# Performance work log

Measured on AMD Instinct MI355X. Metric: run time of the kernel, lower is better.

## Reference

```python
import jax, jax.numpy as jnp
import numpy as np

NMAX = 8
LMAX = 3
RC = 5.0
SMOOTH_WIDTH = 0.5
BASIS_SIGMA = 0.5
N_SPECIES = 4
N_ATOMS = 20000
N_EDGES = 800000
LM = (LMAX + 1) ** 2  # 16


def shifted_cosine_cutoff(r):
    # fc = 1 for r < rc - w; smooth cosine ramp to 0 on [rc - w, rc]; 0 beyond rc
    t = (r - (RC - SMOOTH_WIDTH)) / SMOOTH_WIDTH
    ramp = 0.5 * (jnp.cos(jnp.pi * jnp.clip(t, 0.0, 1.0)) + 1.0)
    return jnp.where(r < RC - SMOOTH_WIDTH, 1.0, jnp.where(r < RC, ramp, 0.0))


def real_sph_harm(v):
    # Real spherical harmonics up to l=3, 'integral' (orthonormal) normalization,
    # e3nn component ordering (l=1 block is y,z,x). v assumed unit vectors. -> (E,16)
    x, y, z = v[:, 0], v[:, 1], v[:, 2]
    x2, y2, z2 = x * x, y * y, z * z
    Y = [
        jnp.full_like(x, 0.28209479177387814),                      # l=0
        0.4886025119029199 * y,                                     # l=1
        0.4886025119029199 * z,
        0.4886025119029199 * x,
        1.0925484305920792 * x * y,                                  # l=2
        1.0925484305920792 * y * z,
        0.31539156525252005 * (3.0 * z2 - 1.0),
        1.0925484305920792 * x * z,
        0.5462742152960396 * (x2 - y2),
        0.5900435899266435 * y * (3.0 * x2 - y2),                   # l=3
        2.890611442640554 * x * y * z,
        0.4570457994644658 * y * (5.0 * z2 - 1.0),
        0.3731763325901154 * z * (5.0 * z2 - 3.0),
        0.4570457994644658 * x * (5.0 * z2 - 1.0),
        1.445305721320277 * z * (x2 - y2),
        0.5900435899266435 * x * (x2 - 3.0 * y2),
    ]
    return jnp.stack(Y, axis=-1)


def setup_inputs() -> dict:
    key = jax.random.key(0)
    k1, k2, k3, k4, k5, k6 = jax.random.split(key, 6)
    distances = jax.random.uniform(k1, (N_EDGES,), dtype=jnp.float32) * RC
    dirs = jax.random.normal(k2, (N_EDGES, 3), dtype=jnp.float32)
    dirs = dirs / jnp.linalg.norm(dirs, axis=1, keepdims=True)
    W_radial = jax.random.normal(k3, (LMAX + 1, NMAX, 16), dtype=jnp.float32)
    centers = jnp.linspace(0.0, RC, 16, dtype=jnp.float32)
    z = jax.random.randint(k4, (N_ATOMS,), 0, N_SPECIES)
    idx_i = jax.random.randint(k5, (N_EDGES,), 0, N_ATOMS)
    idx_j = jax.random.randint(k6, (N_EDGES,), 0, N_ATOMS)
    return {"distances": distances, "direction_vectors": dirs, "W_radial": W_radial,
            "centers": centers, "z": z, "idx_i": idx_i, "idx_j": idx_j}


def reference(distances, direction_vectors, W_radial, centers, z, idx_i, idx_j):
    # radial integrals: splined Rln modeled as linear combo of Gaussian radial basis
    g = jnp.exp(-((distances[:, None] - centers[None, :]) ** 2) / (2.0 * BASIS_SIGMA ** 2))  # (E,K)
    fc = shifted_cosine_cutoff(distances)  # (E,)
    RIln = jnp.einsum('ek,lnk->eln', g, W_radial) * fc[:, None, None]  # (E, lmax+1, nmax)
    Ylm = real_sph_harm(direction_vectors)  # (E, 16)
    # per-l outer product RIln[:,l,:] (x) Ylm block -> (E, nmax, lm)
    blocks = []
    idx = 0
    for l in range(LMAX + 1):
        w = 2 * l + 1
        blocks.append(jnp.einsum('en,em->enm', RIln[:, l, :], Ylm[:, idx:idx + w]))
        idx += w
    cij_nlm = jnp.concatenate(blocks, axis=-1)  # (E, nmax, 16)
    # species-dependent scatter-sum: bin = species_idx(z_j) + n_species * idx_i
    reduction_ids = z[idx_j] + N_SPECIES * idx_i
    ci = jax.ops.segment_sum(cij_nlm, reduction_ids, num_segments=N_SPECIES * N_ATOMS)
    return ci.reshape(N_ATOMS, N_SPECIES, NMAX, LM)
```

## Files before the change

### kernel.cpp

```cpp
#include <hip/hip_runtime.h>


#define NMAXC   8
#define LMC     16
#define NSPECC  4
#define RCUT    5.0f
#define RIN_    4.5f
#define PI_F    3.14159265358979323846f
#define CAP     128
#define CPAD    16

__device__ const int   d_Asel[16] = {0,2,3,1,4,2,0,1,0,2,4,2,3,1,3,1};
__device__ const int   d_Bsel[16] = {0,0,0,0,0,1,2,1,3,4,1,5,6,5,3,7};
__device__ const float d_Clm[16]  = {
    0.28209479177387814f, 0.4886025119029199f, 0.4886025119029199f,
    0.4886025119029199f,  1.0925484305920792f, 1.0925484305920792f,
    0.31539156525252005f, 1.0925484305920792f, 0.5462742152960396f,
    0.5900435899266435f,  2.890611442640554f,  0.4570457994644658f,
    0.3731763325901154f,  0.4570457994644658f, 1.445305721320277f,
    0.5900435899266435f };

__global__ void k_rec_bucket(const float* __restrict__ dist,
                             const float* __restrict__ dirs,
                             const int* __restrict__ zarr,
                             const int* __restrict__ idx_i,
                             const int* __restrict__ idx_j,
                             int* __restrict__ cursors_p,
                             float4* __restrict__ recs, int n_edges) {
    int e = blockIdx.x * blockDim.x + threadIdx.x;
    if (e >= n_edges) return;
    float d = dist[e];
    float x = dirs[3 * e + 0], y = dirs[3 * e + 1], zz = dirs[3 * e + 2];
    int s = zarr[idx_j[e]] & 3;
    int a = idx_i[e];
    int c = atomicAdd(&cursors_p[a * CPAD], 1);
    if (c >= CAP) return;
    unsigned db = (__float_as_uint(d) & ~3u) | (unsigned)s;
    float4 r; r.x = __uint_as_float(db); r.y = x; r.z = y; r.w = zz;
    recs[(size_t)a * CAP + c] = r;
}

__global__ void k_count_p(const int* __restrict__ idx_i, int* __restrict__ counts_p,
                          int n_edges) {
    int e = blockIdx.x * blockDim.x + threadIdx.x;
    if (e < n_edges) atomicAdd(&counts_p[idx_i[e] * CPAD], 1);
}

__global__ __launch_bounds__(1024) void k_scan_p(const int* __restrict__ counts_p,
                                                 int* __restrict__ offsets,
                                                 int* __restrict__ cursors_p, int n) {
    __shared__ int wsum[16];
    __shared__ int carry_s;
    int t = threadIdx.x;
    int lane = t & 63, w = t >> 6;
    if (t == 0) carry_s = 0;
    __syncthreads();
    for (int base = 0; base < n; base += 1024) {
        int i = base + t;
        int v = (i < n) ? counts_p[i * CPAD] : 0;
        int x = v;
        #pragma unroll
        for (int off = 1; off < 64; off <<= 1) {
            int y = __shfl_up(x, off);
            if (lane >= off) x += y;
        }
        if (lane == 63) wsum[w] = x;
        __syncthreads();
        if (w == 0) {
            int ws = (lane < 16) ? wsum[lane] : 0;
            #pragma unroll
            for (int off = 1; off < 16; off <<= 1) {
                int y = __shfl_up(ws, off);
                if (lane >= off) ws += y;
            }
            if (lane < 16) wsum[lane] = ws;
        }
        __syncthreads();
        int wbase = (w > 0) ? wsum[w - 1] : 0;
        int inc = wbase + x;
        int carry = carry_s;
        if (i < n) {
            int exc = carry + inc - v;
            offsets[i] = exc;
            cursors_p[i * CPAD] = exc;
        }
        __syncthreads();
        if (t == 1023) carry_s = carry + inc;
        __syncthreads();
    }
}

__global__ void k_rec_csr(const float* __restrict__ dist,
                          const float* __restrict__ dirs,
                          const int* __restrict__ zarr,
                          const int* __restrict__ idx_i,
                          const int* __restrict__ idx_j,
                          int* __restrict__ cursors_p,
                          float4* __restrict__ recs, int n_edges) {
    int e = blockIdx.x * blockDim.x + threadIdx.x;
    if (e >= n_edges) return;
    float d = dist[e];
    float x = dirs[3 * e + 0], y = dirs[3 * e + 1], zz = dirs[3 * e + 2];
    int s = zarr[idx_j[e]] & 3;
    int a = idx_i[e];
    int c = atomicAdd(&cursors_p[a * CPAD], 1);
    unsigned db = (__float_as_uint(d) & ~3u) | (unsigned)s;
    float4 r; r.x = __uint_as_float(db); r.y = x; r.z = y; r.w = zz;
    recs[c] = r;
}

__global__ __launch_bounds__(128) void k_main(
        const float4* __restrict__ recs, const float* __restrict__ W,
        const float* __restrict__ centers, const int* __restrict__ cnts_p,
        const int* __restrict__ offsets, float* __restrict__ out) {
    const int atom = blockIdx.x;
    const int t = threadIdx.x;
    const int w = t >> 6, L = t & 63;
    const int lm = L & 15;
    const int eL = L >> 4;
    const int l  = (lm >= 9) ? 3 : (lm >= 4) ? 2 : (lm >= 1) ? 1 : 0;
    const int r0 = l * 8 + eL;
    const int row = L & 31, p = L >> 5;

    const float ck   = centers[lm];
    const float c_lm = d_Clm[lm];
    const int   asel = d_Asel[lm], bsel = d_Bsel[lm];

    const float4* wp = reinterpret_cast<const float4*>(W + (row << 4));
    const float4 w0 = wp[0], w1 = wp[1], w2 = wp[2], w3 = wp[3];

    __shared__ float ggfc[2][4][16];
    __shared__ float ylmS[2][4][16];
    __shared__ float rinS[2][4][32];
    __shared__ int   msS [2][4];
    __shared__ float red [2][8][64];

    int cnt = cnts_p[atom * CPAD];
    size_t rbase;
    if (offsets) { rbase = (size_t)offsets[atom]; }
    else         { rbase = (size_t)atom * CAP; if (cnt > CAP) cnt = CAP; }

    float a00 = 0.f, a01 = 0.f, a10 = 0.f, a11 = 0.f;
    float a20 = 0.f, a21 = 0.f, a30 = 0.f, a31 = 0.f;

    for (int base = w * 4; base < cnt; base += 8) {
        int slot = base + eL;
        bool valid = slot < cnt;
        int rs = valid ? slot : base;
        float4 rec = recs[rbase + rs];
        unsigned db = __float_as_uint(rec.x);
        int spec = db & 3;
        float d = rec.x, x = rec.y, y = rec.z, zz = rec.w;
        float tt = fminf(fmaxf((d - RIN_) * 2.0f, 0.0f), 1.0f);
        float fcv = 0.5f * (__cosf(PI_F * tt) + 1.0f);
        float dd = d - ck;
        float g = __expf(-2.0f * dd * dd) * fcv;
        g = valid ? g : 0.0f;
        float x2 = x * x, y2 = y * y, z2 = zz * zz;
        float A = (asel == 0) ? 1.0f :
                  (asel == 1) ? x    :
                  (asel == 2) ? y    :
                  (asel == 3) ? zz   : x * y;
        float B = (bsel == 0) ? 1.0f :
                  (bsel == 1) ? zz   :
                  (bsel == 2) ? fmaf(3.0f, z2, -1.0f) :
                  (bsel == 3) ? (x2 - y2)             :
                  (bsel == 4) ? fmaf(3.0f, x2, -y2)   :
                  (bsel == 5) ? fmaf(5.0f, z2, -1.0f) :
                  (bsel == 6) ? fmaf(5.0f, z2, -3.0f) :
                                fmaf(-3.0f, y2, x2);
        float yv = c_lm * A * B;
        yv = valid ? yv : 0.0f;
        ggfc[w][eL][lm] = g;
        ylmS[w][eL][lm] = yv;
        if (lm == 0) msS[w][eL] = spec;
        __builtin_amdgcn_wave_barrier();
        {
            const float4* ga = reinterpret_cast<const float4*>(&ggfc[w][p][0]);
            const float4* gb = reinterpret_cast<const float4*>(&ggfc[w][p + 2][0]);
            float4 A0 = ga[0], A1 = ga[1], A2 = ga[2], A3 = ga[3];
            float4 B0 = gb[0], B1 = gb[1], B2 = gb[2], B3 = gb[3];
            float ra = A0.x * w0.x;
            ra = fmaf(A0.y, w0.y, ra); ra = fmaf(A0.z, w0.z, ra); ra = fmaf(A0.w, w0.w, ra);
            ra = fmaf(A1.x, w1.x, ra); ra = fmaf(A1.y, w1.y, ra); ra = fmaf(A1.z, w1.z, ra); ra = fmaf(A1.w, w1.w, ra);
            ra = fmaf(A2.x, w2.x, ra); ra = fmaf(A2.y, w2.y, ra); ra = fmaf(A2.z, w2.z, ra); ra = fmaf(A2.w, w2.w, ra);
            ra = fmaf(A3.x, w3.x, ra); ra = fmaf(A3.y, w3.y, ra); ra = fmaf(A3.z, w3.z, ra); ra = fmaf(A3.w, w3.w, ra);
            float rb = B0.x * w0.x;
            rb = fmaf(B0.y, w0.y, rb); rb = fmaf(B0.z, w0.z, rb); rb = fmaf(B0.w, w0.w, rb);
            rb = fmaf(B1.x, w1.x, rb); rb = fmaf(B1.y, w1.y, rb); rb = fmaf(B1.z, w1.z, rb); rb = fmaf(B1.w, w1.w, rb);
            rb = fmaf(B2.x, w2.x, rb); rb = fmaf(B2.y, w2.y, rb); rb = fmaf(B2.z, w2.z, rb); rb = fmaf(B2.w, w2.w, rb);
            rb = fmaf(B3.x, w3.x, rb); rb = fmaf(B3.y, w3.y, rb); rb = fmaf(B3.z, w3.z, rb); rb = fmaf(B3.w, w3.w, rb);
            rinS[w][p][row]     = ra;
            rinS[w][p + 2][row] = rb;
        }
        __builtin_amdgcn_wave_barrier();
        #pragma unroll
        for (int e = 0; e < 4; ++e) {
            float ye = ylmS[w][e][lm];
            float ra = rinS[w][e][r0];
            float rb = rinS[w][e][r0 + 4];
            int s = __builtin_amdgcn_readfirstlane(msS[w][e]);
            float v0 = ra * ye, v1 = rb * ye;
            if (s == 0)      { a00 += v0; a01 += v1; }
            else if (s == 1) { a10 += v0; a11 += v1; }
            else if (s == 2) { a20 += v0; a21 += v1; }
            else             { a30 += v0; a31 += v1; }
        }
        __builtin_amdgcn_wave_barrier();
    }

    red[w][0][L] = a00; red[w][1][L] = a01;
    red[w][2][L] = a10; red[w][3][L] = a11;
    red[w][4][L] = a20; red[w][5][L] = a21;
    red[w][6][L] = a30; red[w][7][L] = a31;
    __syncthreads();
    const int h = t >> 6, Ls = t & 63;
    float* ob = out + (size_t)atom * (NSPECC * NMAXC * LMC);
    #pragma unroll
    for (int s = 0; s < 4; ++s) {
        float v = red[0][s * 2 + h][Ls] + red[1][s * 2 + h][Ls];
        ob[s * 128 + t] = v;
    }
}

__device__ __forceinline__ float cutoff_fn(float d) {
    float tt = (d - RIN_) * 2.0f;
    tt = fminf(fmaxf(tt, 0.0f), 1.0f);
    float ramp = 0.5f * (cosf(PI_F * tt) + 1.0f);
    return (d < RCUT) ? ramp : 0.0f;
}

__device__ __forceinline__ float sph_harm_sw(int lm, float x, float y, float z) {
    float x2 = x * x, y2 = y * y, z2 = z * z;
    switch (lm) {
        case 0:  return 0.28209479177387814f;
        case 1:  return 0.4886025119029199f * y;
        case 2:  return 0.4886025119029199f * z;
        case 3:  return 0.4886025119029199f * x;
        case 4:  return 1.0925484305920792f * x * y;
        case 5:  return 1.0925484305920792f * y * z;
        case 6:  return 0.31539156525252005f * (3.0f * z2 - 1.0f);
        case 7:  return 1.0925484305920792f * x * z;
        case 8:  return 0.5462742152960396f * (x2 - y2);
        case 9:  return 0.5900435899266435f * y * (3.0f * x2 - y2);
        case 10: return 2.890611442640554f * x * y * z;
        case 11: return 0.4570457994644658f * y * (5.0f * z2 - 1.0f);
        case 12: return 0.3731763325901154f * z * (5.0f * z2 - 3.0f);
        case 13: return 0.4570457994644658f * x * (5.0f * z2 - 1.0f);
        case 14: return 1.445305721320277f * z * (x2 - y2);
        default: return 0.5900435899266435f * x * (x2 - 3.0f * y2);
    }
}

__global__ __launch_bounds__(128) void k_atomic(
        const float* __restrict__ distances, const float* __restrict__ dirs,
        const float* __restrict__ W, const float* __restrict__ centers,
        const int* __restrict__ zarr, const int* __restrict__ idx_i,
        const int* __restrict__ idx_j, float* __restrict__ out, int n_edges) {
    const int t = threadIdx.x;
    const int n = t >> 4, lm = t & 15;
    const int base = blockIdx.x * 8;

    __shared__ float4 gbuf[8][4];
    __shared__ float  ylm[8][16];
    __shared__ float  md[8], mfc[8], mx[8], my[8], mz[8];
    __shared__ int    ms[8], mi[8];

    const int l = (lm >= 9) ? 3 : (lm >= 4) ? 2 : (lm >= 1) ? 1 : 0;
    const float4* wp = reinterpret_cast<const float4*>(W + ((l * NMAXC + n) << 4));
    const float4 w0 = wp[0], w1 = wp[1], w2 = wp[2], w3 = wp[3];
    const float ck = centers[lm];

    if (t < 8) {
        int e = base + t;
        if (e < n_edges) {
            float d = distances[e];
            md[t] = d; mfc[t] = cutoff_fn(d);
            mx[t] = dirs[3 * e + 0];
            my[t] = dirs[3 * e + 1];
            mz[t] = dirs[3 * e + 2];
            ms[t] = zarr[idx_j[e]];
            mi[t] = idx_i[e];
        } else {
            md[t] = 1e9f; mfc[t] = 0.f;
            mx[t] = 0.f; my[t] = 0.f; mz[t] = 0.f; ms[t] = 0; mi[t] = 0;
        }
    }
    __syncthreads();
    {
        int e = t >> 4;
        float dd = md[e] - ck;
        reinterpret_cast<float*>(&gbuf[e][0])[lm] = __expf(-2.0f * dd * dd) * mfc[e];
    }
    {
        int e2 = t & 7, lm2 = t >> 3;
        ylm[e2][lm2] = sph_harm_sw(lm2, mx[e2], my[e2], mz[e2]);
    }
    __syncthreads();
    #pragma unroll
    for (int e = 0; e < 8; ++e) {
        float4 a0 = gbuf[e][0], a1 = gbuf[e][1], a2 = gbuf[e][2], a3 = gbuf[e][3];
        float r;
        r = a0.x * w0.x;
        r = fmaf(a0.y, w0.y, r); r = fmaf(a0.z, w0.z, r); r = fmaf(a0.w, w0.w, r);
        r = fmaf(a1.x, w1.x, r); r = fmaf(a1.y, w1.y, r); r = fmaf(a1.z, w1.z, r); r = fmaf(a1.w, w1.w, r);
        r = fmaf(a2.x, w2.x, r); r = fmaf(a2.y, w2.y, r); r = fmaf(a2.z, w2.z, r); r = fmaf(a2.w, w2.w, r);
        r = fmaf(a3.x, w3.x, r); r = fmaf(a3.y, w3.y, r); r = fmaf(a3.z, w3.z, r); r = fmaf(a3.w, w3.w, r);
        float v = r * ylm[e][lm];
        int target = (mi[e] * NSPECC + ms[e]) * (NMAXC * LMC) + t;
        unsafeAtomicAdd(&out[target], v);
    }
}

extern "C" void kernel_launch(void* const* d_in, const int* in_sizes, int n_in,
                              void* d_out, int out_size, void* d_ws, size_t ws_size,
                              hipStream_t stream) {
    const float* distances = (const float*)d_in[0];
    const float* dirs      = (const float*)d_in[1];
    const float* W         = (const float*)d_in[2];
    const float* centers   = (const float*)d_in[3];
    const int*   zarr      = (const int*)d_in[4];
    const int*   idx_i     = (const int*)d_in[5];
    const int*   idx_j     = (const int*)d_in[6];
    float*       out       = (float*)d_out;

    const int n_edges = in_sizes[0];
    const int n_atoms = in_sizes[4];

    const size_t curs_b  = (size_t)n_atoms * CPAD * sizeof(int);
    const size_t need_t1 = curs_b + (size_t)n_atoms * CAP * sizeof(float4) + 64;
    const size_t need_t2 = 2 * curs_b + (size_t)n_atoms * sizeof(int)
                         + (size_t)n_edges * sizeof(float4) + 64;

    if (ws_size >= need_t1) {
        int*    cursors_p = (int*)d_ws;
        float4* recs      = (float4*)((char*)d_ws + curs_b);
        hipMemsetAsync(cursors_p, 0, curs_b, stream);
        k_rec_bucket<<<(n_edges + 255) / 256, 256, 0, stream>>>(
            distances, dirs, zarr, idx_i, idx_j, cursors_p, recs, n_edges);
        k_main<<<n_atoms, 128, 0, stream>>>(recs, W, centers, cursors_p,
                                            nullptr, out);
    } else if (ws_size >= need_t2) {
        int*    counts_p  = (int*)d_ws;
        int*    cursors_p = (int*)((char*)d_ws + curs_b);
        int*    offsets   = (int*)((char*)d_ws + 2 * curs_b);
        float4* recs      = (float4*)((char*)d_ws + 2 * curs_b
                                      + (size_t)n_atoms * sizeof(int));
        hipMemsetAsync(counts_p, 0, curs_b, stream);
        k_count_p<<<(n_edges + 255) / 256, 256, 0, stream>>>(idx_i, counts_p, n_edges);
        k_scan_p<<<1, 1024, 0, stream>>>(counts_p, offsets, cursors_p, n_atoms);
        k_rec_csr<<<(n_edges + 255) / 256, 256, 0, stream>>>(
            distances, dirs, zarr, idx_i, idx_j, cursors_p, recs, n_edges);
        k_main<<<n_atoms, 128, 0, stream>>>(recs, W, centers, counts_p,
                                            offsets, out);
    } else {
        hipMemsetAsync(out, 0, (size_t)out_size * sizeof(float), stream);
        k_atomic<<<(n_edges + 7) / 8, 128, 0, stream>>>(distances, dirs, W, centers,
                                                        zarr, idx_i, idx_j, out, n_edges);
    }
}
```

Before: 198.7 us.

## Split record packing from bucketing; scatter edge ids and prefetch records in main loop

The edge record packing moves into its own coalesced kernel that writes records in edge order, and the bucketing kernel now scatters only 4-byte edge ids per atom instead of 16-byte records. The main kernel reads records indirectly through the id list, handles 8 edges per wave per iteration instead of 4, and prefetches the next records and ids in software. The aim is to shrink the scattered atomic-driven writes and to hide gather latency. The cost is an extra launch, an extra indirection with random 16-byte gathers in the main kernel, and more registers.

Result: slower. 211.7 us (+6.5%).

```diff
diff --git a/kernel.cpp b/kernel.cpp
--- a/kernel.cpp
+++ b/kernel.cpp
@@ -20,24 +20,47 @@
     0.3731763325901154f,  0.4570457994644658f, 1.445305721320277f,
     0.5900435899266435f };
 
-__global__ void k_rec_bucket(const float* __restrict__ dist,
-                             const float* __restrict__ dirs,
-                             const int* __restrict__ zarr,
-                             const int* __restrict__ idx_i,
-                             const int* __restrict__ idx_j,
-                             int* __restrict__ cursors_p,
-                             float4* __restrict__ recs, int n_edges) {
+__device__ __forceinline__ float ylm_eval(int asel, int bsel, float c_lm,
+                                          float x, float y, float zz) {
+    float x2 = x * x, y2 = y * y, z2 = zz * zz;
+    float A = (asel == 0) ? 1.0f :
+              (asel == 1) ? x    :
+              (asel == 2) ? y    :
+              (asel == 3) ? zz   : x * y;
+    float B = (bsel == 0) ? 1.0f :
+              (bsel == 1) ? zz   :
+              (bsel == 2) ? fmaf(3.0f, z2, -1.0f) :
+              (bsel == 3) ? (x2 - y2)             :
+              (bsel == 4) ? fmaf(3.0f, x2, -y2)   :
+              (bsel == 5) ? fmaf(5.0f, z2, -1.0f) :
+              (bsel == 6) ? fmaf(5.0f, z2, -3.0f) :
+                            fmaf(-3.0f, y2, x2);
+    return c_lm * A * B;
+}
+
+__global__ void k_prep(const float* __restrict__ dist,
+                       const float* __restrict__ dirs,
+                       const int* __restrict__ zarr,
+                       const int* __restrict__ idx_j,
+                       float4* __restrict__ recs, int n_edges) {
     int e = blockIdx.x * blockDim.x + threadIdx.x;
     if (e >= n_edges) return;
     float d = dist[e];
     float x = dirs[3 * e + 0], y = dirs[3 * e + 1], zz = dirs[3 * e + 2];
     int s = zarr[idx_j[e]] & 3;
+    unsigned db = (__float_as_uint(d) & ~3u) | (unsigned)s;
+    float4 r; r.x = __uint_as_float(db); r.y = x; r.z = y; r.w = zz;
+    recs[e] = r;
+}
+
+__global__ void k_scatter_id(const int* __restrict__ idx_i,
+                             int* __restrict__ cursors_p,
+                             int* __restrict__ ids, int n_edges) {
+    int e = blockIdx.x * blockDim.x + threadIdx.x;
+    if (e >= n_edges) return;
     int a = idx_i[e];
     int c = atomicAdd(&cursors_p[a * CPAD], 1);
-    if (c >= CAP) return;
-    unsigned db = (__float_as_uint(d) & ~3u) | (unsigned)s;
-    float4 r; r.x = __uint_as_float(db); r.y = x; r.z = y; r.w = zz;
-    recs[(size_t)a * CAP + c] = r;
+    if (c < CAP) ids[a * CAP + c] = e;
 }
 
 __global__ void k_count_p(const int* __restrict__ idx_i, int* __restrict__ counts_p,
@@ -90,123 +113,125 @@
     }
 }
 
-__global__ void k_rec_csr(const float* __restrict__ dist,
-                          const float* __restrict__ dirs,
-                          const int* __restrict__ zarr,
-                          const int* __restrict__ idx_i,
-                          const int* __restrict__ idx_j,
-                          int* __restrict__ cursors_p,
-                          float4* __restrict__ recs, int n_edges) {
+__global__ void k_scatter_id_csr(const int* __restrict__ idx_i,
+                                 int* __restrict__ cursors_p,
+                                 int* __restrict__ ids, int n_edges) {
     int e = blockIdx.x * blockDim.x + threadIdx.x;
     if (e >= n_edges) return;
-    float d = dist[e];
-    float x = dirs[3 * e + 0], y = dirs[3 * e + 1], zz = dirs[3 * e + 2];
-    int s = zarr[idx_j[e]] & 3;
-    int a = idx_i[e];
-    int c = atomicAdd(&cursors_p[a * CPAD], 1);
-    unsigned db = (__float_as_uint(d) & ~3u) | (unsigned)s;
-    float4 r; r.x = __uint_as_float(db); r.y = x; r.z = y; r.w = zz;
-    recs[c] = r;
+    int pos = atomicAdd(&cursors_p[idx_i[e] * CPAD], 1);
+    ids[pos] = e;
 }
 
 __global__ __launch_bounds__(128) void k_main(
-        const float4* __restrict__ recs, const float* __restrict__ W,
-        const float* __restrict__ centers, const int* __restrict__ cnts_p,
-        const int* __restrict__ offsets, float* __restrict__ out) {
+        const float4* __restrict__ recs, const int* __restrict__ ids_all,
+        const float* __restrict__ W, const float* __restrict__ centers,
+        const int* __restrict__ cnts_p, const int* __restrict__ offsets,
+        float* __restrict__ out) {
     const int atom = blockIdx.x;
     const int t = threadIdx.x;
     const int w = t >> 6, L = t & 63;
-    const int lm = L & 15;
-    const int eL = L >> 4;
+    const int lm = L & 15, g = L >> 4;
     const int l  = (lm >= 9) ? 3 : (lm >= 4) ? 2 : (lm >= 1) ? 1 : 0;
-    const int r0 = l * 8 + eL;
+    const int r0 = l * 8 + g;
     const int row = L & 31, p = L >> 5;
 
     const float ck   = centers[lm];
     const float c_lm = d_Clm[lm];
     const int   asel = d_Asel[lm], bsel = d_Bsel[lm];
-
     const float4* wp = reinterpret_cast<const float4*>(W + (row << 4));
     const float4 w0 = wp[0], w1 = wp[1], w2 = wp[2], w3 = wp[3];
 
-    __shared__ float ggfc[2][4][16];
-    __shared__ float ylmS[2][4][16];
-    __shared__ float rinS[2][4][32];
-    __shared__ int   msS [2][4];
+    __shared__ float ggfc[2][8][16];
+    __shared__ float ylmS[2][8][16];
+    __shared__ float rinS[2][8][32];
+    __shared__ int   msS [2][8];
     __shared__ float red [2][8][64];
 
     int cnt = cnts_p[atom * CPAD];
-    size_t rbase;
-    if (offsets) { rbase = (size_t)offsets[atom]; }
-    else         { rbase = (size_t)atom * CAP; if (cnt > CAP) cnt = CAP; }
-
-    float a00 = 0.f, a01 = 0.f, a10 = 0.f, a11 = 0.f;
-    float a20 = 0.f, a21 = 0.f, a30 = 0.f, a31 = 0.f;
-
-    for (int base = w * 4; base < cnt; base += 8) {
-        int slot = base + eL;
-        bool valid = slot < cnt;
-        int rs = valid ? slot : base;
-        float4 rec = recs[rbase + rs];
-        unsigned db = __float_as_uint(rec.x);
-        int spec = db & 3;
-        float d = rec.x, x = rec.y, y = rec.z, zz = rec.w;
-        float tt = fminf(fmaxf((d - RIN_) * 2.0f, 0.0f), 1.0f);
-        float fcv = 0.5f * (__cosf(PI_F * tt) + 1.0f);
-        float dd = d - ck;
-        float g = __expf(-2.0f * dd * dd) * fcv;
-        g = valid ? g : 0.0f;
-        float x2 = x * x, y2 = y * y, z2 = zz * zz;
-        float A = (asel == 0) ? 1.0f :
-                  (asel == 1) ? x    :
-                  (asel == 2) ? y    :
-                  (asel == 3) ? zz   : x * y;
-        float B = (bsel == 0) ? 1.0f :
-                  (bsel == 1) ? zz   :
-                  (bsel == 2) ? fmaf(3.0f, z2, -1.0f) :
-                  (bsel == 3) ? (x2 - y2)             :
-                  (bsel == 4) ? fmaf(3.0f, x2, -y2)   :
-                  (bsel == 5) ? fmaf(5.0f, z2, -1.0f) :
-                  (bsel == 6) ? fmaf(5.0f, z2, -3.0f) :
-                                fmaf(-3.0f, y2, x2);
-        float yv = c_lm * A * B;
-        yv = valid ? yv : 0.0f;
-        ggfc[w][eL][lm] = g;
-        ylmS[w][eL][lm] = yv;
-        if (lm == 0) msS[w][eL] = spec;
-        __builtin_amdgcn_wave_barrier();
-        {
-            const float4* ga = reinterpret_cast<const float4*>(&ggfc[w][p][0]);
-            const float4* gb = reinterpret_cast<const float4*>(&ggfc[w][p + 2][0]);
-            float4 A0 = ga[0], A1 = ga[1], A2 = ga[2], A3 = ga[3];
-            float4 B0 = gb[0], B1 = gb[1], B2 = gb[2], B3 = gb[3];
-            float ra = A0.x * w0.x;
-            ra = fmaf(A0.y, w0.y, ra); ra = fmaf(A0.z, w0.z, ra); ra = fmaf(A0.w, w0.w, ra);
-            ra = fmaf(A1.x, w1.x, ra); ra = fmaf(A1.y, w1.y, ra); ra = fmaf(A1.z, w1.z, ra); ra = fmaf(A1.w, w1.w, ra);
-            ra = fmaf(A2.x, w2.x, ra); ra = fmaf(A2.y, w2.y, ra); ra = fmaf(A2.z, w2.z, ra); ra = fmaf(A2.w, w2.w, ra);
-            ra = fmaf(A3.x, w3.x, ra); ra = fmaf(A3.y, w3.y, ra); ra = fmaf(A3.z, w3.z, ra); ra = fmaf(A3.w, w3.w, ra);
-            float rb = B0.x * w0.x;
-            rb = fmaf(B0.y, w0.y, rb); rb = fmaf(B0.z, w0.z, rb); rb = fmaf(B0.w, w0.w, rb);
-            rb = fmaf(B1.x, w1.x, rb); rb = fmaf(B1.y, w1.y, rb); rb = fmaf(B1.z, w1.z, rb); rb = fmaf(B1.w, w1.w, rb);
-            rb = fmaf(B2.x, w2.x, rb); rb = fmaf(B2.y, w2.y, rb); rb = fmaf(B2.z, w2.z, rb); rb = fmaf(B2.w, w2.w, rb);
-            rb = fmaf(B3.x, w3.x, rb); rb = fmaf(B3.y, w3.y, rb); rb = fmaf(B3.z, w3.z, rb); rb = fmaf(B3.w, w3.w, rb);
-            rinS[w][p][row]     = ra;
-            rinS[w][p + 2][row] = rb;
-        }
-        __builtin_amdgcn_wave_barrier();
-        #pragma unroll
-        for (int e = 0; e < 4; ++e) {
-            float ye = ylmS[w][e][lm];
-            float ra = rinS[w][e][r0];
-            float rb = rinS[w][e][r0 + 4];
-            int s = __builtin_amdgcn_readfirstlane(msS[w][e]);
-            float v0 = ra * ye, v1 = rb * ye;
-            if (s == 0)      { a00 += v0; a01 += v1; }
-            else if (s == 1) { a10 += v0; a11 += v1; }
-            else if (s == 2) { a20 += v0; a21 += v1; }
-            else             { a30 += v0; a31 += v1; }
-        }
-        __builtin_amdgcn_wave_barrier();
+    const int* idsp;
+    if (offsets) { idsp = ids_all + offsets[atom]; }
+    else { idsp = ids_all + (size_t)atom * CAP; if (cnt > CAP) cnt = CAP; }
+
+    float a00=0.f,a01=0.f,a10=0.f,a11=0.f,a20=0.f,a21=0.f,a30=0.f,a31=0.f;
+
+    if (cnt > 0) {
+        int base = w * 8;
+        int sA = base + g, sB = sA + 4;
+        bool vA = sA < cnt, vB = sB < cnt;
+        int iA = idsp[vA ? sA : 0];
+        int iB = idsp[vB ? sB : 0];
+        int sA1 = sA + 16, sB1 = sB + 16;
+        bool vA1 = sA1 < cnt, vB1 = sB1 < cnt;
+        int iA1 = idsp[vA1 ? sA1 : 0];
+        int iB1 = idsp[vB1 ? sB1 : 0];
+        float4 rA = recs[iA], rB = recs[iB];
+
+        for (; base < cnt; base += 16) {
+            float4 rAn = recs[iA1], rBn = recs[iB1];
+            int sA2 = sA + 32, sB2 = sB + 32;
+            bool vA2 = sA2 < cnt, vB2 = sB2 < cnt;
+            int iA2 = idsp[vA2 ? sA2 : 0];
+            int iB2 = idsp[vB2 ? sB2 : 0];
+
+            {
+                float d = rA.x, x = rA.y, y = rA.z, zz = rA.w;
+                int spec = __float_as_uint(d) & 3;
+                float tt = fminf(fmaxf((d - RIN_) * 2.0f, 0.0f), 1.0f);
+                float fcv = 0.5f * (__cosf(PI_F * tt) + 1.0f);
+                float dd = d - ck;
+                float gv = __expf(-2.0f * dd * dd) * fcv;
+                gv = vA ? gv : 0.0f;
+                float yv = ylm_eval(asel, bsel, c_lm, x, y, zz);
+                yv = vA ? yv : 0.0f;
+                ggfc[w][g][lm] = gv; ylmS[w][g][lm] = yv;
+                if (lm == 0) msS[w][g] = spec;
+            }
+            {
+                float d = rB.x, x = rB.y, y = rB.z, zz = rB.w;
+                int spec = __float_as_uint(d) & 3;
+                float tt = fminf(fmaxf((d - RIN_) * 2.0f, 0.0f), 1.0f);
+                float fcv = 0.5f * (__cosf(PI_F * tt) + 1.0f);
+                float dd = d - ck;
+                float gv = __expf(-2.0f * dd * dd) * fcv;
+                gv = vB ? gv : 0.0f;
+                float yv = ylm_eval(asel, bsel, c_lm, x, y, zz);
+                yv = vB ? yv : 0.0f;
+                ggfc[w][g + 4][lm] = gv; ylmS[w][g + 4][lm] = yv;
+                if (lm == 0) msS[w][g + 4] = spec;
+            }
+            __builtin_amdgcn_wave_barrier();
+            #pragma unroll
+            for (int q = 0; q < 4; ++q) {
+                int e = p + 2 * q;
+                const float4* ga = reinterpret_cast<const float4*>(&ggfc[w][e][0]);
+                float4 A0 = ga[0], A1 = ga[1], A2 = ga[2], A3 = ga[3];
+                float r = A0.x * w0.x;
+                r = fmaf(A0.y, w0.y, r); r = fmaf(A0.z, w0.z, r); r = fmaf(A0.w, w0.w, r);
+                r = fmaf(A1.x, w1.x, r); r = fmaf(A1.y, w1.y, r); r = fmaf(A1.z, w1.z, r); r = fmaf(A1.w, w1.w, r);
+                r = fmaf(A2.x, w2.x, r); r = fmaf(A2.y, w2.y, r); r = fmaf(A2.z, w2.z, r); r = fmaf(A2.w, w2.w, r);
+                r = fmaf(A3.x, w3.x, r); r = fmaf(A3.y, w3.y, r); r = fmaf(A3.z, w3.z, r); r = fmaf(A3.w, w3.w, r);
+                rinS[w][e][row] = r;
+            }
+            __builtin_amdgcn_wave_barrier();
+            #pragma unroll
+            for (int e = 0; e < 8; ++e) {
+                float ye = ylmS[w][e][lm];
+                float va = rinS[w][e][r0];
+                float vb = rinS[w][e][r0 + 4];
+                int s = __builtin_amdgcn_readfirstlane(msS[w][e]);
+                float v0 = va * ye, v1 = vb * ye;
+                if (s == 0)      { a00 += v0; a01 += v1; }
+                else if (s == 1) { a10 += v0; a11 += v1; }
+                else if (s == 2) { a20 += v0; a21 += v1; }
+                else             { a30 += v0; a31 += v1; }
+            }
+            __builtin_amdgcn_wave_barrier();
+
+            rA = rAn; rB = rBn;
+            vA = vA1; vB = vB1;
+            sA = sA1; sB = sB1;
+            sA1 = sA2; sB1 = sB2; vA1 = vA2; vB1 = vB2; iA1 = iA2; iB1 = iB2;
+        }
     }
 
     red[w][0][L] = a00; red[w][1][L] = a01;
@@ -217,10 +242,8 @@
     const int h = t >> 6, Ls = t & 63;
     float* ob = out + (size_t)atom * (NSPECC * NMAXC * LMC);
     #pragma unroll
-    for (int s = 0; s < 4; ++s) {
-        float v = red[0][s * 2 + h][Ls] + red[1][s * 2 + h][Ls];
-        ob[s * 128 + t] = v;
-    }
+    for (int s = 0; s < 4; ++s)
+        ob[s * 128 + t] = red[0][s * 2 + h][Ls] + red[1][s * 2 + h][Ls];
 }
 
 __device__ __forceinline__ float cutoff_fn(float d) {
@@ -228,28 +251,6 @@
     tt = fminf(fmaxf(tt, 0.0f), 1.0f);
     float ramp = 0.5f * (cosf(PI_F * tt) + 1.0f);
     return (d < RCUT) ? ramp : 0.0f;
-}
-
-__device__ __forceinline__ float sph_harm_sw(int lm, float x, float y, float z) {
-    float x2 = x * x, y2 = y * y, z2 = z * z;
-    switch (lm) {
-        case 0:  return 0.28209479177387814f;
-        case 1:  return 0.4886025119029199f * y;
-        case 2:  return 0.4886025119029199f * z;
-        case 3:  return 0.4886025119029199f * x;
-        case 4:  return 1.0925484305920792f * x * y;
-        case 5:  return 1.0925484305920792f * y * z;
-        case 6:  return 0.31539156525252005f * (3.0f * z2 - 1.0f);
-        case 7:  return 1.0925484305920792f * x * z;
-        case 8:  return 0.5462742152960396f * (x2 - y2);
-        case 9:  return 0.5900435899266435f * y * (3.0f * x2 - y2);
-        case 10: return 2.890611442640554f * x * y * z;
-        case 11: return 0.4570457994644658f * y * (5.0f * z2 - 1.0f);
-        case 12: return 0.3731763325901154f * z * (5.0f * z2 - 3.0f);
-        case 13: return 0.4570457994644658f * x * (5.0f * z2 - 1.0f);
-        case 14: return 1.445305721320277f * z * (x2 - y2);
-        default: return 0.5900435899266435f * x * (x2 - 3.0f * y2);
-    }
 }
 
 __global__ __launch_bounds__(128) void k_atomic(
@@ -294,7 +295,8 @@
     }
     {
         int e2 = t & 7, lm2 = t >> 3;
-        ylm[e2][lm2] = sph_harm_sw(lm2, mx[e2], my[e2], mz[e2]);
+        ylm[e2][lm2] = ylm_eval(d_Asel[lm2], d_Bsel[lm2], d_Clm[lm2],
+                                mx[e2], my[e2], mz[e2]);
     }
     __syncthreads();
     #pragma unroll
@@ -326,32 +328,38 @@
 
     const int n_edges = in_sizes[0];
     const int n_atoms = in_sizes[4];
-
-    const size_t curs_b  = (size_t)n_atoms * CPAD * sizeof(int);
-    const size_t need_t1 = curs_b + (size_t)n_atoms * CAP * sizeof(float4) + 64;
-    const size_t need_t2 = 2 * curs_b + (size_t)n_atoms * sizeof(int)
-                         + (size_t)n_edges * sizeof(float4) + 64;
+    const int eb = (n_edges + 255) / 256;
+
+    const size_t curs_b = (size_t)n_atoms * CPAD * sizeof(int);
+    const size_t recs_b = (size_t)n_edges * sizeof(float4);
+    const size_t ids1_b = (size_t)n_atoms * CAP * sizeof(int);
+    const size_t ids2_b = (size_t)n_edges * sizeof(int);
+    const size_t offs_b = (size_t)n_atoms * sizeof(int);
+
+    const size_t need_t1 = curs_b + ids1_b + recs_b + 64;
+    const size_t need_t2 = 2 * curs_b + offs_b + ids2_b + recs_b + 64;
 
     if (ws_size >= need_t1) {
         int*    cursors_p = (int*)d_ws;
-        float4* recs      = (float4*)((char*)d_ws + curs_b);
+        int*    ids       = (int*)((char*)d_ws + curs_b);
+        float4* recs      = (float4*)((char*)d_ws + curs_b + ids1_b);
         hipMemsetAsync(cursors_p, 0, curs_b, stream);
-        k_rec_bucket<<<(n_edges + 255) / 256, 256, 0, stream>>>(
-            distances, dirs, zarr, idx_i, idx_j, cursors_p, recs, n_edges);
-        k_main<<<n_atoms, 128, 0, stream>>>(recs, W, centers, cursors_p,
+        k_prep<<<eb, 256, 0, stream>>>(distances, dirs, zarr, idx_j, recs, n_edges);
+        k_scatter_id<<<eb, 256, 0, stream>>>(idx_i, cursors_p, ids, n_edges);
+        k_main<<<n_atoms, 128, 0, stream>>>(recs, ids, W, centers, cursors_p,
                                             nullptr, out);
     } else if (ws_size >= need_t2) {
         int*    counts_p  = (int*)d_ws;
         int*    cursors_p = (int*)((char*)d_ws + curs_b);
         int*    offsets   = (int*)((char*)d_ws + 2 * curs_b);
-        float4* recs      = (float4*)((char*)d_ws + 2 * curs_b
-                                      + (size_t)n_atoms * sizeof(int));
+        int*    ids       = (int*)((char*)d_ws + 2 * curs_b + offs_b);
+        float4* recs      = (float4*)((char*)d_ws + 2 * curs_b + offs_b + ids2_b);
         hipMemsetAsync(counts_p, 0, curs_b, stream);
-        k_count_p<<<(n_edges + 255) / 256, 256, 0, stream>>>(idx_i, counts_p, n_edges);
+        k_prep<<<eb, 256, 0, stream>>>(distances, dirs, zarr, idx_j, recs, n_edges);
+        k_count_p<<<eb, 256, 0, stream>>>(idx_i, counts_p, n_edges);
         k_scan_p<<<1, 1024, 0, stream>>>(counts_p, offsets, cursors_p, n_atoms);
-        k_rec_csr<<<(n_edges + 255) / 256, 256, 0, stream>>>(
-            distances, dirs, zarr, idx_i, idx_j, cursors_p, recs, n_edges);
-        k_main<<<n_atoms, 128, 0, stream>>>(recs, W, centers, counts_p,
+        k_scatter_id_csr<<<eb, 256, 0, stream>>>(idx_i, cursors_p, ids, n_edges);
+        k_main<<<n_atoms, 128, 0, stream>>>(recs, ids, W, centers, counts_p,
                                             offsets, out);
     } else {
         hipMemsetAsync(out, 0, (size_t)out_size * sizeof(float), stream);
```
